# Performance work log

Hardware: AMD Instinct MI355X
Metric: run time of the kernel (lower is better)

The kernel has to match this reference:

```python
import jax, jax.numpy as jnp
from jax import lax
import numpy as np

B, L, D, KSIZE = 8, 2048, 256, 8


def setup_inputs() -> dict:
    key = jax.random.key(0)
    kx, kw, kwin, kb, ktau = jax.random.split(key, 5)
    scale = 1.0 / np.sqrt(D).astype(np.float32)
    x = jax.random.normal(kx, (B, L, D), dtype=jnp.float32)
    weight = jax.random.normal(kw, (D, D), dtype=jnp.float32) * scale
    input_weight = jax.random.normal(kwin, (D, D), dtype=jnp.float32) * scale
    bias = jax.random.normal(kb, (1, D), dtype=jnp.float32)
    # tau = |randn| in the original; offset by 1 to keep 1/tau numerically sane
    tau = jnp.abs(jax.random.normal(ktau, (1, D), dtype=jnp.float32)) + 1.0
    return {"x": x, "weight": weight, "input_weight": input_weight,
            "bias": bias, "tau": tau, "ksize": KSIZE}


def reference(x, weight, input_weight, bias, tau, ksize):
    b, l, d = x.shape
    # get_K: left-pad with (ksize-1) zeros, gather overlapping windows
    xp = jnp.pad(x, ((0, 0), (ksize - 1, 0), (0, 0)))
    idx = jnp.arange(l)[:, None] + jnp.arange(ksize)[None, :]  # (l, ksize)
    windows = xp[:, idx, :]                                    # (b, l, ksize, d)
    xw = windows.reshape(b * l, ksize, d)                      # flatten per-window batch

    inv_tau = 1.0 / tau                                        # (1, d)
    h0 = jnp.zeros((b * l, d), dtype=x.dtype)

    def step(h, xt):
        # SimpleCTRNN update: h += (1/tau) * (-h + relu(h W + x W_in + b))
        h_new = h + inv_tau * (-h + jax.nn.relu(h @ weight + xt @ input_weight + bias))
        return h_new, None

    xs = jnp.swapaxes(xw, 0, 1)                                # (ksize, b*l, d)
    h_last, _ = lax.scan(step, h0, xs)
    # forward() keeps only the last window timestep
    return h_last.reshape(b, l, d)
```

## Files before the change

### kernel.cpp

```cpp
#include <hip/hip_runtime.h>

typedef __bf16 bf16_t;
typedef __bf16 bf16x8 __attribute__((ext_vector_type(8)));
typedef float  f32x4  __attribute__((ext_vector_type(4)));

#define Ldim 2048
#define Ddim 256

__global__ void swz_kernel(const float* __restrict__ w,
                           const float* __restrict__ win,
                           bf16_t* __restrict__ wsw,
                           bf16_t* __restrict__ winsw) {
    int mat = blockIdx.x >> 3, kt = blockIdx.x & 7;
    const float* src = mat ? win : w;
    bf16_t*      dst = mat ? winsw : wsw;
    int ln = threadIdx.x & 63, g = threadIdx.x >> 6;
    int c = ln & 15, q = ln >> 4;
#pragma unroll
    for (int i = 0; i < 4; ++i) {
        int nt = g + 4 * i;
        bf16x8 v;
#pragma unroll
        for (int j = 0; j < 8; ++j)
            v[j] = (bf16_t)src[(kt * 32 + q * 8 + j) * Ddim + nt * 16 + c];
        *(bf16x8*)&dst[((kt * 16 + nt) * 64 + ln) * 8] = v;
    }
}

#define AU_STRIDE 258
#define AU_ROWS   40
#define AU_BYTES  (AU_ROWS * AU_STRIDE * 4)
#define HBUF_BYTES 32768
#define LDS_TOTAL (HBUF_BYTES + AU_BYTES)

extern __shared__ char ldsmem[];

__global__ __launch_bounds__(256, 2)
void rnn_kernel(const float* __restrict__ x,
                const float* __restrict__ bias,
                const float* __restrict__ tau,
                const bf16x8* __restrict__ wsw,
                const bf16x8* __restrict__ winsw,
                float* __restrict__ out)
{
    char*  hb  = ldsmem;
    float* auf = (float*)(ldsmem + HBUF_BYTES);

    const int tid = threadIdx.x;
    const int w   = tid >> 6;
    const int ln  = tid & 63;
    const int c   = ln & 15;
    const int q   = ln >> 4;
    const int tile = blockIdx.x;
    const int bb  = tile >> 6;
    const int l0  = (tile & 63) * 32;

    int   ncol[4];
    float itau[4];
#pragma unroll
    for (int nl = 0; nl < 4; ++nl) {
        ncol[nl] = (w * 4 + nl) * 16 + c;
        itau[nl] = 1.0f / tau[ncol[nl]];
    }

    f32x4 au[3][4];
#pragma unroll
    for (int nl = 0; nl < 4; ++nl) {
        float bv = bias[ncol[nl]];
#pragma unroll
        for (int mt = 0; mt < 3; ++mt) {
            f32x4 t = {bv, bv, bv, bv};
            au[mt][nl] = t;
        }
    }

    const float* xb = x + (long)bb * (Ldim * Ddim);
    const f32x4 zf = {0.f, 0.f, 0.f, 0.f};

    auto loadX = [&](f32x4 (&buf)[3][2], int kt) {
#pragma unroll
        for (int mt = 0; mt < 3; ++mt) {
            int  lrow = l0 - 7 + mt * 16 + c;
            bool ok   = (lrow >= 0) && (lrow < Ldim);
            const f32x4* p = (const f32x4*)(xb + (long)lrow * Ddim + kt * 32 + q * 8);
            buf[mt][0] = ok ? p[0] : zf;
            buf[mt][1] = ok ? p[1] : zf;
        }
    };
    auto loadW = [&](bf16x8 (&wb)[4], int kt) {
#pragma unroll
        for (int nl = 0; nl < 4; ++nl)
            wb[nl] = winsw[(kt * 16 + 4 * w + nl) * 64 + ln];
    };
    auto step1 = [&](const f32x4 (&buf)[3][2], const bf16x8 (&wb)[4]) {
        bf16x8 aF[3];
#pragma unroll
        for (int mt = 0; mt < 3; ++mt)
#pragma unroll
            for (int jj = 0; jj < 4; ++jj) {
                aF[mt][jj]     = (bf16_t)buf[mt][0][jj];
                aF[mt][jj + 4] = (bf16_t)buf[mt][1][jj];
            }
#pragma unroll
        for (int nl = 0; nl < 4; ++nl)
#pragma unroll
            for (int mt = 0; mt < 3; ++mt)
                au[mt][nl] = __builtin_amdgcn_mfma_f32_16x16x32_bf16(
                    aF[mt], wb[nl], au[mt][nl], 0, 0, 0);
    };

    {
        f32x4  x0[3][2], x1[3][2];
        bf16x8 w0[4], w1[4];
        loadX(x0, 0); loadW(w0, 0);
#pragma unroll 1
        for (int kk = 0; kk < 4; ++kk) {
            loadX(x1, 2 * kk + 1); loadW(w1, 2 * kk + 1);
            step1(x0, w0);
            if (kk < 3) { loadX(x0, 2 * kk + 2); loadW(w0, 2 * kk + 2); }
            step1(x1, w1);
        }
    }

#pragma unroll
    for (int mt = 0; mt < 3; ++mt)
#pragma unroll
        for (int nl = 0; nl < 4; ++nl)
#pragma unroll
            for (int r = 0; r < 4; ++r) {
                int row = mt * 16 + q * 4 + r;
                if (row < 39)
                    auf[row * AU_STRIDE + ncol[nl]] = au[mt][nl][r];
            }

    f32x4 h[2][4];
#pragma unroll
    for (int mt = 0; mt < 2; ++mt)
#pragma unroll
        for (int nl = 0; nl < 4; ++nl)
#pragma unroll
            for (int r = 0; r < 4; ++r)
                h[mt][nl][r] = itau[nl] * fmaxf(au[mt][nl][r], 0.0f);

    bf16x8 bfr[8][4];
#pragma unroll
    for (int kt = 0; kt < 8; ++kt)
#pragma unroll
        for (int nl = 0; nl < 4; ++nl)
            bfr[kt][nl] = wsw[(kt * 16 + 4 * w + nl) * 64 + ln];

    int offn[4];
#pragma unroll
    for (int nl = 0; nl < 4; ++nl) {
        int kk = ncol[nl];
        offn[nl] = (kk >> 5) * 1024 + ((kk >> 3) & 3) * 64 + q * 16 + (kk & 7) * 2;
    }
    const int permln = (((ln & 3) << 4) | ((ln >> 4) << 2) | ((ln >> 2) & 3)) * 16;

#pragma unroll
    for (int mt = 0; mt < 2; ++mt)
#pragma unroll
        for (int nl = 0; nl < 4; ++nl)
#pragma unroll
            for (int r = 0; r < 4; ++r)
                *(bf16_t*)(hb + mt * 8192 + r * 256 + offn[nl]) =
                    (bf16_t)h[mt][nl][r];

    const float* ub[4];
#pragma unroll
    for (int nl = 0; nl < 4; ++nl)
        ub[nl] = auf + (4 * q + 1) * AU_STRIDE + ncol[nl];

    float up[2][4][4];
#pragma unroll
    for (int mt = 0; mt < 2; ++mt)
#pragma unroll
        for (int nl = 0; nl < 4; ++nl)
#pragma unroll
            for (int r = 0; r < 4; ++r)
                up[mt][nl][r] = ub[nl][(mt * 16 + r) * AU_STRIDE];

    __syncthreads();

    int cur = 0;
#pragma unroll 1
    for (int t = 1; t < 8; ++t) {
        char* pc = hb + cur * 16384 + permln;
        char* pn = hb + (cur ^ 1) * 16384;
#pragma unroll
        for (int mt = 0; mt < 2; ++mt) {
            f32x4 acc[4];
#pragma unroll
            for (int nl = 0; nl < 4; ++nl) {
                f32x4 a = {up[mt][nl][0], up[mt][nl][1], up[mt][nl][2], up[mt][nl][3]};
                acc[nl] = a;
            }
            if (mt == 1 && t < 7) {
#pragma unroll
                for (int nl = 0; nl < 4; ++nl) ub[nl] += AU_STRIDE;
#pragma unroll
                for (int m2 = 0; m2 < 2; ++m2)
#pragma unroll
                    for (int nl = 0; nl < 4; ++nl)
#pragma unroll
                        for (int r = 0; r < 4; ++r)
                            up[m2][nl][r] = ub[nl][(m2 * 16 + r) * AU_STRIDE];
            }
            __builtin_amdgcn_s_setprio(1);
#pragma unroll
            for (int kt = 0; kt < 8; ++kt) {
                bf16x8 aF = *(const bf16x8*)(pc + (mt * 8 + kt) * 1024);
#pragma unroll
                for (int nl = 0; nl < 4; ++nl)
                    acc[nl] = __builtin_amdgcn_mfma_f32_16x16x32_bf16(
                        aF, bfr[kt][nl], acc[nl], 0, 0, 0);
            }
            __builtin_amdgcn_s_setprio(0);
#pragma unroll
            for (int nl = 0; nl < 4; ++nl)
#pragma unroll
                for (int r = 0; r < 4; ++r) {
                    float hh = h[mt][nl][r];
                    float s  = fmaxf(acc[nl][r], 0.0f);
                    hh = hh + itau[nl] * (s - hh);
                    h[mt][nl][r] = hh;
                    if (t < 7)
                        *(bf16_t*)(pn + mt * 8192 + r * 256 + offn[nl]) = (bf16_t)hh;
                }
        }
        if (t < 7) __syncthreads();
        cur ^= 1;
    }

    float* ob = out + ((long)bb * Ldim + l0) * Ddim;
#pragma unroll
    for (int mt = 0; mt < 2; ++mt)
#pragma unroll
        for (int nl = 0; nl < 4; ++nl)
#pragma unroll
            for (int r = 0; r < 4; ++r)
                ob[(mt * 16 + 4 * q + r) * Ddim + ncol[nl]] = h[mt][nl][r];
}

extern "C" void kernel_launch(void* const* d_in, const int* in_sizes, int n_in,
                              void* d_out, int out_size, void* d_ws, size_t ws_size,
                              hipStream_t stream) {
    const float* x            = (const float*)d_in[0];
    const float* weight       = (const float*)d_in[1];
    const float* input_weight = (const float*)d_in[2];
    const float* bias         = (const float*)d_in[3];
    const float* tau          = (const float*)d_in[4];
    (void)in_sizes; (void)n_in; (void)out_size; (void)ws_size;

    bf16_t* wsw   = (bf16_t*)d_ws;
    bf16_t* winsw = wsw + 65536;

    static bool attr_set = false;
    if (!attr_set) {
        (void)hipFuncSetAttribute((const void*)rnn_kernel,
                                  hipFuncAttributeMaxDynamicSharedMemorySize,
                                  LDS_TOTAL);
        attr_set = true;
    }

    swz_kernel<<<16, 256, 0, stream>>>(weight, input_weight, wsw, winsw);
    rnn_kernel<<<512, 256, LDS_TOTAL, stream>>>(x, bias, tau,
                                                (const bf16x8*)wsw,
                                                (const bf16x8*)winsw,
                                                (float*)d_out);
}
```

Before: 108.0 us.

## Stage shared x rows in LDS so each wave reads 32 rows once

Before, each of the four waves loaded all 48 x rows per k-tile from global memory, so the same data was fetched four times. Now the first 32 rows of the input tile are loaded cooperatively once, written to LDS, and read back by every wave. Only the last 16-row sub-tile is still loaded from global per wave, with prefetch. This aims to cut redundant global and L2 traffic in the input projection, at the cost of an extra barrier, LDS reads, and front-loaded loads that wait before the MFMA work starts.

After: 104.6 us. -3.2%, faster.

```diff
diff --git a/kernel.cpp b/kernel.cpp
--- a/kernel.cpp
+++ b/kernel.cpp
@@ -31,6 +31,7 @@
 #define AU_ROWS   40
 #define AU_BYTES  (AU_ROWS * AU_STRIDE * 4)
 #define HBUF_BYTES 32768
+#define XS_BYTES   32768
 #define LDS_TOTAL (HBUF_BYTES + AU_BYTES)
 
 extern __shared__ char ldsmem[];
@@ -44,6 +45,7 @@
                 float* __restrict__ out)
 {
     char*  hb  = ldsmem;
+    char*  xs  = ldsmem + HBUF_BYTES;
     float* auf = (float*)(ldsmem + HBUF_BYTES);
 
     const int tid = threadIdx.x;
@@ -63,6 +65,35 @@
         itau[nl] = 1.0f / tau[ncol[nl]];
     }
 
+    const float* xb = x + (long)bb * (Ldim * Ddim);
+    const f32x4 zf = {0.f, 0.f, 0.f, 0.f};
+
+    f32x4 sv[8];
+    int   sfl[8];
+#pragma unroll
+    for (int it = 0; it < 8; ++it) {
+        int flat = it * 4 + w;
+        sfl[it] = flat;
+        int mt = flat >> 4, kt = (flat >> 1) & 7, hh = flat & 1;
+        int lrow = l0 - 7 + mt * 16 + c;
+        int rcl  = lrow < 0 ? 0 : lrow;
+        const f32x4* g = (const f32x4*)(xb + (long)rcl * Ddim + kt * 32 + q * 8 + hh * 4);
+        f32x4 v = *g;
+        sv[it] = (lrow >= 0) ? v : zf;
+    }
+
+    bf16x8 w0[4], w1[4];
+    auto loadW = [&](bf16x8 (&wb)[4], int kt) {
+#pragma unroll
+        for (int nl = 0; nl < 4; ++nl)
+            wb[nl] = winsw[(kt * 16 + 4 * w + nl) * 64 + ln];
+    };
+    loadW(w0, 0); loadW(w1, 1);
+
+#pragma unroll
+    for (int it = 0; it < 8; ++it)
+        *(f32x4*)(xs + sfl[it] * 1024 + ln * 16) = sv[it];
+
     f32x4 au[3][4];
 #pragma unroll
     for (int nl = 0; nl < 4; ++nl) {
@@ -74,33 +105,30 @@
         }
     }
 
-    const float* xb = x + (long)bb * (Ldim * Ddim);
-    const f32x4 zf = {0.f, 0.f, 0.f, 0.f};
-
-    auto loadX = [&](f32x4 (&buf)[3][2], int kt) {
-#pragma unroll
-        for (int mt = 0; mt < 3; ++mt) {
-            int  lrow = l0 - 7 + mt * 16 + c;
-            bool ok   = (lrow >= 0) && (lrow < Ldim);
-            const f32x4* p = (const f32x4*)(xb + (long)lrow * Ddim + kt * 32 + q * 8);
-            buf[mt][0] = ok ? p[0] : zf;
-            buf[mt][1] = ok ? p[1] : zf;
-        }
+    auto loadXg = [&](f32x4 (&buf)[2], int kt) {
+        int  lrow = l0 + 25 + c;
+        bool ok   = lrow < Ldim;
+        const f32x4* p = (const f32x4*)(xb + (long)lrow * Ddim + kt * 32 + q * 8);
+        buf[0] = ok ? p[0] : zf;
+        buf[1] = ok ? p[1] : zf;
     };
-    auto loadW = [&](bf16x8 (&wb)[4], int kt) {
-#pragma unroll
-        for (int nl = 0; nl < 4; ++nl)
-            wb[nl] = winsw[(kt * 16 + 4 * w + nl) * 64 + ln];
-    };
-    auto step1 = [&](const f32x4 (&buf)[3][2], const bf16x8 (&wb)[4]) {
+    auto step1 = [&](int kt, const f32x4 (&xg)[2], const bf16x8 (&wb)[4]) {
         bf16x8 aF[3];
 #pragma unroll
-        for (int mt = 0; mt < 3; ++mt)
+        for (int mt = 0; mt < 2; ++mt) {
+            f32x4 b0 = *(const f32x4*)(xs + (mt * 16 + kt * 2 + 0) * 1024 + ln * 16);
+            f32x4 b1 = *(const f32x4*)(xs + (mt * 16 + kt * 2 + 1) * 1024 + ln * 16);
 #pragma unroll
             for (int jj = 0; jj < 4; ++jj) {
-                aF[mt][jj]     = (bf16_t)buf[mt][0][jj];
-                aF[mt][jj + 4] = (bf16_t)buf[mt][1][jj];
-            }
+                aF[mt][jj]     = (bf16_t)b0[jj];
+                aF[mt][jj + 4] = (bf16_t)b1[jj];
+            }
+        }
+#pragma unroll
+        for (int jj = 0; jj < 4; ++jj) {
+            aF[2][jj]     = (bf16_t)xg[0][jj];
+            aF[2][jj + 4] = (bf16_t)xg[1][jj];
+        }
 #pragma unroll
         for (int nl = 0; nl < 4; ++nl)
 #pragma unroll
@@ -110,17 +138,20 @@
     };
 
     {
-        f32x4  x0[3][2], x1[3][2];
-        bf16x8 w0[4], w1[4];
-        loadX(x0, 0); loadW(w0, 0);
+        f32x4 xg0[2], xg1[2];
+        loadXg(xg0, 0);
+        __syncthreads();
+        loadXg(xg1, 1);
 #pragma unroll 1
         for (int kk = 0; kk < 4; ++kk) {
-            loadX(x1, 2 * kk + 1); loadW(w1, 2 * kk + 1);
-            step1(x0, w0);
-            if (kk < 3) { loadX(x0, 2 * kk + 2); loadW(w0, 2 * kk + 2); }
-            step1(x1, w1);
-        }
-    }
+            step1(2 * kk, xg0, w0);
+            if (kk < 3) { loadXg(xg0, 2 * kk + 2); loadW(w0, 2 * kk + 2); }
+            step1(2 * kk + 1, xg1, w1);
+            if (kk < 3) { loadXg(xg1, 2 * kk + 3); loadW(w1, 2 * kk + 3); }
+        }
+    }
+
+    __syncthreads();
 
 #pragma unroll
     for (int mt = 0; mt < 3; ++mt)
```
